# Kernel tuning notes

Hardware: AMD Instinct MI355X
Metric: run time of the kernel (lower is better)

Reference implementation:

```python
import jax, jax.numpy as jnp
import numpy as np

B, S, D, H = 2, 2048, 1024, 16
DK = D // H


def setup_inputs() -> dict:
    key = jax.random.key(0)
    ks = jax.random.split(key, 12)
    scale = 1.0 / np.sqrt(D)
    inp = {
        "q": jax.random.normal(ks[0], (B, S, D), dtype=jnp.float32),
        "k": jax.random.normal(ks[1], (B, S, D), dtype=jnp.float32),
        "v": jax.random.normal(ks[2], (B, S, D), dtype=jnp.float32),
        # causal mask, broadcast over batch and heads; 0 -> masked
        "mask": jnp.tril(jnp.ones((S, S), dtype=jnp.int32))[None, None, :, :],
        "wq_w": jax.random.normal(ks[3], (D, D), dtype=jnp.float32) * scale,
        "wq_b": jax.random.normal(ks[4], (D,), dtype=jnp.float32) * scale,
        "wk_w": jax.random.normal(ks[5], (D, D), dtype=jnp.float32) * scale,
        "wk_b": jax.random.normal(ks[6], (D,), dtype=jnp.float32) * scale,
        "wv_w": jax.random.normal(ks[7], (D, D), dtype=jnp.float32) * scale,
        "wv_b": jax.random.normal(ks[8], (D,), dtype=jnp.float32) * scale,
        "wo_w": jax.random.normal(ks[9], (D, D), dtype=jnp.float32) * scale,
        "wo_b": jax.random.normal(ks[10], (D,), dtype=jnp.float32) * scale,
    }
    return inp


def _split_heads(x):
    b, s, _ = x.shape
    return x.reshape(b, s, H, DK).transpose(0, 2, 1, 3)  # [B,H,S,DK]


def reference(q, k, v, mask, wq_w, wq_b, wk_w, wk_b, wv_w, wv_b, wo_w, wo_b):
    Q = _split_heads(q @ wq_w.T + wq_b)
    K = _split_heads(k @ wk_w.T + wk_b)
    V = _split_heads(v @ wv_w.T + wv_b)
    scale = 1.0 / jnp.sqrt(jnp.asarray(DK, dtype=Q.dtype))
    scores = jnp.einsum("bhqd,bhkd->bhqk", Q, K) * scale  # [B,H,S,S]
    scores = jnp.where(mask == 0, jnp.asarray(-1e9, dtype=scores.dtype), scores)
    attn = jax.nn.softmax(scores, axis=-1)
    out = jnp.einsum("bhqk,bhkd->bhqd", attn, V)  # [B,H,S,DK]
    out = out.transpose(0, 2, 1, 3).reshape(out.shape[0], -1, D)  # [B,S,D]
    return out @ wo_w.T + wo_b
```

## Files before the change

### kernel.cpp

```cpp
#include <hip/hip_runtime.h>
#include <hip/hip_bf16.h>

#define B_ 2
#define S_ 2048
#define D_ 1024
#define H_ 16
#define DK_ 64
#define M_ (B_*S_)

typedef __bf16 bf16;
typedef __bf16 bf16x8 __attribute__((ext_vector_type(8)));
typedef __bf16 bf16x4 __attribute__((ext_vector_type(4)));
typedef float  f32x4  __attribute__((ext_vector_type(4)));

#define GLOAD_LDS16(gp, lp) __builtin_amdgcn_global_load_lds( \
    (const __attribute__((address_space(1))) void*)(gp),      \
    (__attribute__((address_space(3))) void*)(lp), 16, 0, 0)

__global__ __launch_bounds__(256) void cast_kernel(
    const float* __restrict__ q, const float* __restrict__ k, const float* __restrict__ v,
    const float* __restrict__ wq, const float* __restrict__ wk,
    const float* __restrict__ wv, const float* __restrict__ wo,
    bf16* __restrict__ dst)
{
  const size_t XN = (size_t)M_ * D_;
  const size_t WN = (size_t)D_ * D_;
  size_t e = ((size_t)blockIdx.x * 256 + threadIdx.x) * 8;
  const float* src; size_t off;
  if (e < XN)        { src = q; off = e; }
  else if (e < 2*XN) { src = k; off = e - XN; }
  else if (e < 3*XN) { src = v; off = e - 2*XN; }
  else {
    size_t w = e - 3*XN; size_t wi = w >> 20; off = w & (WN - 1);
    src = (wi == 0) ? wq : (wi == 1) ? wk : (wi == 2) ? wv : wo;
  }
  float4 a = *reinterpret_cast<const float4*>(src + off);
  float4 b = *reinterpret_cast<const float4*>(src + off + 4);
  bf16x8 o;
  o[0]=(bf16)a.x; o[1]=(bf16)a.y; o[2]=(bf16)a.z; o[3]=(bf16)a.w;
  o[4]=(bf16)b.x; o[5]=(bf16)b.y; o[6]=(bf16)b.z; o[7]=(bf16)b.w;
  *reinterpret_cast<bf16x8*>(dst + e) = o;
}

__device__ __forceinline__ void gemm_mainloop_128(
    const bf16* __restrict__ A, const bf16* __restrict__ W,
    int m0, int n0, int Kdim, bf16* As, bf16* Bs, f32x4 acc[4][4])
{
  const int tid  = threadIdx.x;
  const int lane = tid & 63;
  const int wave = tid >> 6;
  const int wr   = wave >> 1;
  const int wc   = wave & 1;
  const int g    = lane >> 4;
  const int c    = lane & 15;

#pragma unroll
  for (int i = 0; i < 4; ++i)
#pragma unroll
    for (int j = 0; j < 4; ++j)
      acc[i][j] = (f32x4){0.f, 0.f, 0.f, 0.f};

  for (int kt = 0; kt < Kdim; kt += 32) {
    __syncthreads();
#pragma unroll
    for (int u = 0; u < 2; ++u) {
      int ch  = tid + u*256;
      int row = ch >> 2;
      int col = (ch & 3) * 8;
      GLOAD_LDS16(A + (size_t)(m0 + row)*Kdim + kt + col, As + ch*8);
      GLOAD_LDS16(W + (size_t)(n0 + row)*Kdim + kt + col, Bs + ch*8);
    }
    __syncthreads();

    bf16x8 af[4], bw[4];
#pragma unroll
    for (int i = 0; i < 4; ++i)
      af[i] = *reinterpret_cast<const bf16x8*>(As + (wr*64 + i*16 + c)*32 + g*8);
#pragma unroll
    for (int j = 0; j < 4; ++j)
      bw[j] = *reinterpret_cast<const bf16x8*>(Bs + (wc*64 + j*16 + c)*32 + g*8);
#pragma unroll
    for (int i = 0; i < 4; ++i)
#pragma unroll
      for (int j = 0; j < 4; ++j)
        acc[i][j] = __builtin_amdgcn_mfma_f32_16x16x32_bf16(af[i], bw[j], acc[i][j], 0, 0, 0);
  }
}

__global__ __launch_bounds__(256) void gemm_qkv_kernel(
    const bf16* __restrict__ X, const bf16* __restrict__ Wb,
    const float* __restrict__ bq, const float* __restrict__ bk, const float* __restrict__ bv,
    bf16* __restrict__ Qo, bf16* __restrict__ Ko, bf16* __restrict__ Vo)
{
  __shared__ bf16 As[128*32];
  __shared__ bf16 Bs[128*32];
  const int z  = blockIdx.z;
  const int m0 = blockIdx.y * 128;
  const int n0 = blockIdx.x * 128;
  const bf16* A = X  + (size_t)z * ((size_t)M_ * D_);
  const bf16* W = Wb + (size_t)z * ((size_t)D_ * D_);
  const float* bias = (z == 0) ? bq : (z == 1) ? bk : bv;

  f32x4 acc[4][4];
  gemm_mainloop_128(A, W, m0, n0, D_, As, Bs, acc);

  const int lane = threadIdx.x & 63;
  const int wave = threadIdx.x >> 6;
  const int wr = wave >> 1, wc = wave & 1;
  const int g = lane >> 4,  c = lane & 15;
  bf16* dstQK = (z == 0) ? Qo : Ko;

#pragma unroll
  for (int i = 0; i < 4; ++i) {
#pragma unroll
    for (int j = 0; j < 4; ++j) {
      const int n  = n0 + wc*64 + j*16 + c;
      const float bn = bias[n];
      const int h = n >> 6, dk = n & 63;
      const int mrow = m0 + wr*64 + i*16 + g*4;
      if (z == 2) {
        const int b = mrow >> 11, s = mrow & 2047;
        bf16x4 pv;
#pragma unroll
        for (int r = 0; r < 4; ++r) pv[r] = (bf16)(acc[i][j][r] + bn);
        *reinterpret_cast<bf16x4*>(Vo + ((size_t)((b*H_ + h)*DK_ + dk))*S_ + s) = pv;
      } else {
#pragma unroll
        for (int r = 0; r < 4; ++r) {
          const int m = mrow + r;
          const int b = m >> 11, s = m & 2047;
          dstQK[((size_t)((b*H_ + h)*S_ + s))*DK_ + dk] = (bf16)(acc[i][j][r] + bn);
        }
      }
    }
  }
}

__global__ __launch_bounds__(256) void gemm_out_kernel(
    const bf16* __restrict__ A, const bf16* __restrict__ W,
    const float* __restrict__ bias, float* __restrict__ out)
{
  __shared__ bf16 As[128*32];
  __shared__ bf16 Bs[128*32];
  const int m0 = blockIdx.y * 128;
  const int n0 = blockIdx.x * 128;

  f32x4 acc[4][4];
  gemm_mainloop_128(A, W, m0, n0, D_, As, Bs, acc);

  const int lane = threadIdx.x & 63;
  const int wave = threadIdx.x >> 6;
  const int wr = wave >> 1, wc = wave & 1;
  const int g = lane >> 4,  c = lane & 15;

#pragma unroll
  for (int i = 0; i < 4; ++i) {
#pragma unroll
    for (int j = 0; j < 4; ++j) {
      const int n = n0 + wc*64 + j*16 + c;
      const float bn = bias[n];
      const int mrow = m0 + wr*64 + i*16 + g*4;
#pragma unroll
      for (int r = 0; r < 4; ++r)
        out[(size_t)(mrow + r)*D_ + n] = acc[i][j][r] + bn;
    }
  }
}

__global__ __launch_bounds__(256) void attn_kernel(
    const bf16* __restrict__ Q, const bf16* __restrict__ K,
    const bf16* __restrict__ Vt, bf16* __restrict__ O)
{
  const int qt   = (int)gridDim.x - 1 - (int)blockIdx.x;
  const int bh   = blockIdx.y;
  const int b    = bh >> 4;
  const int hh   = bh & 15;
  const int q0   = qt * 128;
  const int tid  = threadIdx.x;
  const int wave = tid >> 6;
  const int lane = tid & 63;
  const int g    = lane >> 4;
  const int c    = lane & 15;

  __shared__ bf16 Kt_lds[64*64];
  __shared__ bf16 Vt_lds[64*64];
  __shared__ bf16 P_lds[4][32*64];

  const bf16* Qh = Q  + (size_t)bh * (S_*DK_);
  const bf16* Kh = K  + (size_t)bh * (S_*DK_);
  const bf16* Vh = Vt + (size_t)bh * (DK_*S_);

  const int qw0 = q0 + wave*32;

  bf16x8 qfrag[2][2];
#pragma unroll
  for (int qf = 0; qf < 2; ++qf)
#pragma unroll
    for (int ch = 0; ch < 2; ++ch)
      qfrag[qf][ch] = *reinterpret_cast<const bf16x8*>(
          Qh + (size_t)(qw0 + qf*16 + c)*DK_ + ch*32 + g*8);

  f32x4 o_[2][4];
#pragma unroll
  for (int qf = 0; qf < 2; ++qf)
#pragma unroll
    for (int d = 0; d < 4; ++d)
      o_[qf][d] = (f32x4){0.f, 0.f, 0.f, 0.f};
  float m_st[2] = {-1e30f, -1e30f};
  float l_st[2] = {0.f, 0.f};

  const float SC = 0.18033688011112042f;

  const int ntiles = q0/64 + 2;
  const int qmaxw  = qw0 + 31;

  for (int t = 0; t < ntiles; ++t) {
    const int kv0 = t * 64;
    __syncthreads();
#pragma unroll
    for (int u = 0; u < 2; ++u) {
      int ch  = tid + u*256;
      int row = ch >> 3;
      int ssl = (ch & 7) ^ (row & 7);
      GLOAD_LDS16(Kh + (size_t)(kv0 + row)*DK_ + ssl*8, Kt_lds + ch*8);
      GLOAD_LDS16(Vh + (size_t)row*S_ + kv0 + ssl*8,    Vt_lds + ch*8);
    }
    __syncthreads();

    if (kv0 <= qmaxw) {
      f32x4 st[4][2];
#pragma unroll
      for (int kvf = 0; kvf < 4; ++kvf)
#pragma unroll
        for (int qf = 0; qf < 2; ++qf)
          st[kvf][qf] = (f32x4){0.f, 0.f, 0.f, 0.f};

#pragma unroll
      for (int kvf = 0; kvf < 4; ++kvf) {
        const int kvr = kvf*16 + c;
        bf16x8 kf[2];
#pragma unroll
        for (int ch = 0; ch < 2; ++ch) {
          int off = kvr*128 + (((ch*4 + g) ^ (kvr & 7)) << 4);
          kf[ch] = *reinterpret_cast<const bf16x8*>(
              reinterpret_cast<const char*>(Kt_lds) + off);
        }
#pragma unroll
        for (int qf = 0; qf < 2; ++qf)
#pragma unroll
          for (int ch = 0; ch < 2; ++ch)
            st[kvf][qf] = __builtin_amdgcn_mfma_f32_16x16x32_bf16(
                kf[ch], qfrag[qf][ch], st[kvf][qf], 0, 0, 0);
      }

#pragma unroll
      for (int qf = 0; qf < 2; ++qf) {
        const int qrow = qw0 + qf*16 + c;
        float mloc = -1e30f;
#pragma unroll
        for (int kvf = 0; kvf < 4; ++kvf)
#pragma unroll
          for (int r = 0; r < 4; ++r) {
            const int kv = kv0 + kvf*16 + g*4 + r;
            float vv = st[kvf][qf][r] * SC;
            vv = (kv <= qrow) ? vv : -1e30f;
            st[kvf][qf][r] = vv;
            mloc = fmaxf(mloc, vv);
          }
        mloc = fmaxf(mloc, __shfl_xor(mloc, 16));
        mloc = fmaxf(mloc, __shfl_xor(mloc, 32));
        const float mnew = fmaxf(m_st[qf], mloc);
        const float corr = exp2f(m_st[qf] - mnew);
        float lsum = 0.f;
        const int q_l = qf*16 + c;
#pragma unroll
        for (int kvf = 0; kvf < 4; ++kvf) {
          bf16x4 pb;
#pragma unroll
          for (int r = 0; r < 4; ++r) {
            float p = exp2f(st[kvf][qf][r] - mnew);
            lsum += p;
            pb[r] = (bf16)p;
          }
          int wb = (q_l*128 + kvf*32 + g*8) ^ ((q_l & 7) << 4);
          *reinterpret_cast<bf16x4*>(reinterpret_cast<char*>(P_lds[wave]) + wb) = pb;
        }
        lsum += __shfl_xor(lsum, 16);
        lsum += __shfl_xor(lsum, 32);
        l_st[qf] = l_st[qf]*corr + lsum;
        m_st[qf] = mnew;
#pragma unroll
        for (int r = 0; r < 4; ++r) {
          float rc = __shfl(corr, (lane & 48) | (g*4 + r));
#pragma unroll
          for (int d = 0; d < 4; ++d)
            o_[qf][d][r] *= rc;
        }
      }

      bf16x8 pf[2][2];
#pragma unroll
      for (int qf = 0; qf < 2; ++qf) {
        const int q_l = qf*16 + c;
#pragma unroll
        for (int ch = 0; ch < 2; ++ch) {
          int rb = (q_l*128 + ch*64 + g*16) ^ ((q_l & 7) << 4);
          pf[qf][ch] = *reinterpret_cast<const bf16x8*>(
              reinterpret_cast<const char*>(P_lds[wave]) + rb);
        }
      }
#pragma unroll
      for (int d = 0; d < 4; ++d) {
        const int dkr = d*16 + c;
#pragma unroll
        for (int ch = 0; ch < 2; ++ch) {
          int vb = dkr*128 + (((ch*4 + g) ^ (dkr & 7)) << 4);
          bf16x8 vf = *reinterpret_cast<const bf16x8*>(
              reinterpret_cast<const char*>(Vt_lds) + vb);
#pragma unroll
          for (int qf = 0; qf < 2; ++qf)
            o_[qf][d] = __builtin_amdgcn_mfma_f32_16x16x32_bf16(
                pf[qf][ch], vf, o_[qf][d], 0, 0, 0);
        }
      }
    }
  }

#pragma unroll
  for (int qf = 0; qf < 2; ++qf) {
    const float linv = 1.f / l_st[qf];
#pragma unroll
    for (int r = 0; r < 4; ++r) {
      const float li = __shfl(linv, (lane & 48) | (g*4 + r));
      const int qrow = qw0 + qf*16 + g*4 + r;
      bf16* orow = O + ((size_t)(b*S_ + qrow)*H_ + hh)*DK_;
#pragma unroll
      for (int d = 0; d < 4; ++d)
        orow[d*16 + c] = (bf16)(o_[qf][d][r] * li);
    }
  }
}

extern "C" void kernel_launch(void* const* d_in, const int* in_sizes, int n_in,
                              void* d_out, int out_size, void* d_ws, size_t ws_size,
                              hipStream_t stream)
{
  const float* q    = (const float*)d_in[0];
  const float* k    = (const float*)d_in[1];
  const float* v    = (const float*)d_in[2];
  const float* wq_w = (const float*)d_in[4];
  const float* wq_b = (const float*)d_in[5];
  const float* wk_w = (const float*)d_in[6];
  const float* wk_b = (const float*)d_in[7];
  const float* wv_w = (const float*)d_in[8];
  const float* wv_b = (const float*)d_in[9];
  const float* wo_w = (const float*)d_in[10];
  const float* wo_b = (const float*)d_in[11];

  const size_t XN = (size_t)M_ * D_;
  const size_t WN = (size_t)D_ * D_;
  bf16* ws  = (bf16*)d_ws;
  bf16* xq  = ws;
  bf16* wqb = ws + 3*XN;
  bf16* Qs  = wqb + 4*WN;
  bf16* Ks  = Qs + XN;
  bf16* Vts = Ks + XN;
  bf16* Os  = ws;

  cast_kernel<<<dim3(8192), dim3(256), 0, stream>>>(q, k, v, wq_w, wk_w, wv_w, wo_w, xq);
  gemm_qkv_kernel<<<dim3(8, 32, 3), dim3(256), 0, stream>>>(
      xq, wqb, wq_b, wk_b, wv_b, Qs, Ks, Vts);
  attn_kernel<<<dim3(16, 32), dim3(256), 0, stream>>>(Qs, Ks, Vts, Os);
  gemm_out_kernel<<<dim3(8, 32), dim3(256), 0, stream>>>(Os, wqb + 3*WN, wo_b, (float*)d_out);
}
```

Before: 285.4 us.

## Rewrite attention with 32x32 MFMA, register-resident P, and double-buffered KV

Reworks the attention kernel to use 32x32x16 MFMA tiles, with each lane owning one query row. The softmax probabilities are repacked into MFMA operands with cross-lane shuffles instead of a round trip through LDS. K/V tiles are double-buffered so the next tile's global-to-LDS load overlaps the current compute, leaving one barrier per iteration. The softmax scale is folded into the Q projection epilogue, the causal masking is skipped for tiles fully below the diagonal, and a launch bound of two blocks per unit is set. In exchange it doubles LDS for K/V and uses a finite -30000 mask value.

After: 267.7 us. 6.2% less time.

```diff
diff --git a/kernel.cpp b/kernel.cpp
--- a/kernel.cpp
+++ b/kernel.cpp
@@ -11,11 +11,19 @@
 typedef __bf16 bf16;
 typedef __bf16 bf16x8 __attribute__((ext_vector_type(8)));
 typedef __bf16 bf16x4 __attribute__((ext_vector_type(4)));
+typedef __bf16 bf16x2 __attribute__((ext_vector_type(2)));
 typedef float  f32x4  __attribute__((ext_vector_type(4)));
+typedef float  f32x16 __attribute__((ext_vector_type(16)));
+typedef int    i32x4  __attribute__((ext_vector_type(4)));
 
 #define GLOAD_LDS16(gp, lp) __builtin_amdgcn_global_load_lds( \
     (const __attribute__((address_space(1))) void*)(gp),      \
     (__attribute__((address_space(3))) void*)(lp), 16, 0, 0)
+
+static __device__ __forceinline__ int packbf(float a, float b) {
+  bf16x2 t; t[0] = (bf16)a; t[1] = (bf16)b;
+  return __builtin_bit_cast(int, t);
+}
 
 __global__ __launch_bounds__(256) void cast_kernel(
     const float* __restrict__ q, const float* __restrict__ k, const float* __restrict__ v,
@@ -100,6 +108,7 @@
   const bf16* A = X  + (size_t)z * ((size_t)M_ * D_);
   const bf16* W = Wb + (size_t)z * ((size_t)D_ * D_);
   const float* bias = (z == 0) ? bq : (z == 1) ? bk : bv;
+  const float sc = (z == 0) ? 0.18033688011112042f : 1.0f;
 
   f32x4 acc[4][4];
   gemm_mainloop_128(A, W, m0, n0, D_, As, Bs, acc);
@@ -129,7 +138,7 @@
         for (int r = 0; r < 4; ++r) {
           const int m = mrow + r;
           const int b = m >> 11, s = m & 2047;
-          dstQK[((size_t)((b*H_ + h)*S_ + s))*DK_ + dk] = (bf16)(acc[i][j][r] + bn);
+          dstQK[((size_t)((b*H_ + h)*S_ + s))*DK_ + dk] = (bf16)((acc[i][j][r] + bn) * sc);
         }
       }
     }
@@ -167,7 +176,7 @@
   }
 }
 
-__global__ __launch_bounds__(256) void attn_kernel(
+__global__ __launch_bounds__(256, 2) void attn_kernel(
     const bf16* __restrict__ Q, const bf16* __restrict__ K,
     const bf16* __restrict__ Vt, bf16* __restrict__ O)
 {
@@ -179,166 +188,150 @@
   const int tid  = threadIdx.x;
   const int wave = tid >> 6;
   const int lane = tid & 63;
-  const int g    = lane >> 4;
-  const int c    = lane & 15;
-
-  __shared__ bf16 Kt_lds[64*64];
-  __shared__ bf16 Vt_lds[64*64];
-  __shared__ bf16 P_lds[4][32*64];
+  const int ql   = lane & 31;
+  const int hi   = lane >> 5;
+
+  const float NEG = -30000.0f;
+
+  __shared__ bf16 Kl[2][64*64];
+  __shared__ bf16 Vl[2][64*64];
 
   const bf16* Qh = Q  + (size_t)bh * (S_*DK_);
   const bf16* Kh = K  + (size_t)bh * (S_*DK_);
   const bf16* Vh = Vt + (size_t)bh * (DK_*S_);
 
-  const int qw0 = q0 + wave*32;
-
-  bf16x8 qfrag[2][2];
-#pragma unroll
-  for (int qf = 0; qf < 2; ++qf)
-#pragma unroll
-    for (int ch = 0; ch < 2; ++ch)
-      qfrag[qf][ch] = *reinterpret_cast<const bf16x8*>(
-          Qh + (size_t)(qw0 + qf*16 + c)*DK_ + ch*32 + g*8);
-
-  f32x4 o_[2][4];
-#pragma unroll
-  for (int qf = 0; qf < 2; ++qf)
-#pragma unroll
-    for (int d = 0; d < 4; ++d)
-      o_[qf][d] = (f32x4){0.f, 0.f, 0.f, 0.f};
-  float m_st[2] = {-1e30f, -1e30f};
-  float l_st[2] = {0.f, 0.f};
-
-  const float SC = 0.18033688011112042f;
-
-  const int ntiles = q0/64 + 2;
-  const int qmaxw  = qw0 + 31;
-
-  for (int t = 0; t < ntiles; ++t) {
+  const int qw0  = q0 + wave*32;
+  const int qrow = qw0 + ql;
+
+  bf16x8 qf[4];
+#pragma unroll
+  for (int ck = 0; ck < 4; ++ck)
+    qf[ck] = *reinterpret_cast<const bf16x8*>(Qh + (size_t)qrow*DK_ + ck*16 + hi*8);
+
+  f32x16 o0 = {}, o1 = {};
+  float m_ = 0.f, l_ = 0.f;
+
+  const int nt = q0/64 + 2;
+
+#define STAGE_KV(kv0s, bb) do {                                              \
+  _Pragma("unroll")                                                          \
+  for (int u = 0; u < 2; ++u) {                                              \
+    int ch  = tid + u*256;                                                   \
+    int row = ch >> 3;                                                       \
+    int g   = (ch & 7) ^ (row & 7);            \
+    GLOAD_LDS16(Kh + (size_t)((kv0s) + row)*DK_ + g*8, &Kl[bb][ch*8]);       \
+    GLOAD_LDS16(Vh + (size_t)row*S_ + (kv0s) + g*8,    &Vl[bb][ch*8]);       \
+  }                                                                          \
+} while (0)
+
+#define MK_PA(dst, s, base) do {                                               \
+    int x0 = packbf(s[(base)+0], s[(base)+1]);                                 \
+    int x1 = packbf(s[(base)+2], s[(base)+3]);                                 \
+    int y0 = packbf(s[(base)+4], s[(base)+5]);                                 \
+    int y1 = packbf(s[(base)+6], s[(base)+7]);                                 \
+    int px0 = __shfl_xor(x0, 32), px1 = __shfl_xor(x1, 32);                    \
+    int py0 = __shfl_xor(y0, 32), py1 = __shfl_xor(y1, 32);                    \
+    i32x4 w;                                                                   \
+    w[0] = hi ? py0 : x0;  w[1] = hi ? py1 : x1;                               \
+    w[2] = hi ? y0  : px0; w[3] = hi ? y1  : px1;                              \
+    dst = __builtin_bit_cast(bf16x8, w);                                       \
+  } while (0)
+
+  int cur = 0;
+  STAGE_KV(0, 0);
+  __syncthreads();
+
+  for (int t = 0; t < nt; ++t) {
     const int kv0 = t * 64;
+    if (t + 1 < nt) STAGE_KV((t+1)*64, cur ^ 1);
+
+    if (kv0 <= qw0 + 31) {
+      const char* Kb = (const char*)Kl[cur];
+      const char* Vb = (const char*)Vl[cur];
+
+      f32x16 st0 = {}, st1 = {};
+#pragma unroll
+      for (int ck = 0; ck < 4; ++ck) {
+        bf16x8 kf0 = *reinterpret_cast<const bf16x8*>(
+            Kb + ql*128 + (((ck*2 + hi) ^ (ql & 7)) << 4));
+        st0 = __builtin_amdgcn_mfma_f32_32x32x16_bf16(kf0, qf[ck], st0, 0, 0, 0);
+        bf16x8 kf1 = *reinterpret_cast<const bf16x8*>(
+            Kb + (32 + ql)*128 + (((ck*2 + hi) ^ (ql & 7)) << 4));
+        st1 = __builtin_amdgcn_mfma_f32_32x32x16_bf16(kf1, qf[ck], st1, 0, 0, 0);
+      }
+
+      if (kv0 + 63 > qw0) {
+#pragma unroll
+        for (int r = 0; r < 16; ++r) {
+          const int kvr = kv0 + (r & 3) + 8*(r >> 2) + 4*hi;
+          st0[r] = (kvr      <= qrow) ? st0[r] : NEG;
+          st1[r] = (kvr + 32 <= qrow) ? st1[r] : NEG;
+        }
+      }
+
+      float pm = st0[0];
+#pragma unroll
+      for (int r = 1; r < 16; ++r) pm = fmaxf(pm, st0[r]);
+#pragma unroll
+      for (int r = 0; r < 16; ++r) pm = fmaxf(pm, st1[r]);
+      pm = fmaxf(pm, __shfl_xor(pm, 32));
+
+      const float mnew = fmaxf(m_, pm);
+      const float corr = exp2f(m_ - mnew);
+      m_ = mnew;
+
+      float ls = 0.f;
+#pragma unroll
+      for (int r = 0; r < 16; ++r) {
+        float p = exp2f(st0[r] - mnew);
+        ls += p;
+        st0[r] = p;
+      }
+#pragma unroll
+      for (int r = 0; r < 16; ++r) {
+        float p = exp2f(st1[r] - mnew);
+        ls += p;
+        st1[r] = p;
+      }
+      l_ = l_ * corr + (ls + __shfl_xor(ls, 32));
+      o0 *= corr; o1 *= corr;
+
+      bf16x8 pa[4];
+      MK_PA(pa[0], st0, 0);
+      MK_PA(pa[1], st0, 8);
+      MK_PA(pa[2], st1, 0);
+      MK_PA(pa[3], st1, 8);
+
+#pragma unroll
+      for (int ck = 0; ck < 4; ++ck) {
+        bf16x8 vf0 = *reinterpret_cast<const bf16x8*>(
+            Vb + ql*128 + (((ck*2 + hi) ^ (ql & 7)) << 4));
+        o0 = __builtin_amdgcn_mfma_f32_32x32x16_bf16(vf0, pa[ck], o0, 0, 0, 0);
+        bf16x8 vf1 = *reinterpret_cast<const bf16x8*>(
+            Vb + (32 + ql)*128 + (((ck*2 + hi) ^ (ql & 7)) << 4));
+        o1 = __builtin_amdgcn_mfma_f32_32x32x16_bf16(vf1, pa[ck], o1, 0, 0, 0);
+      }
+    }
+
     __syncthreads();
-#pragma unroll
-    for (int u = 0; u < 2; ++u) {
-      int ch  = tid + u*256;
-      int row = ch >> 3;
-      int ssl = (ch & 7) ^ (row & 7);
-      GLOAD_LDS16(Kh + (size_t)(kv0 + row)*DK_ + ssl*8, Kt_lds + ch*8);
-      GLOAD_LDS16(Vh + (size_t)row*S_ + kv0 + ssl*8,    Vt_lds + ch*8);
-    }
-    __syncthreads();
-
-    if (kv0 <= qmaxw) {
-      f32x4 st[4][2];
-#pragma unroll
-      for (int kvf = 0; kvf < 4; ++kvf)
-#pragma unroll
-        for (int qf = 0; qf < 2; ++qf)
-          st[kvf][qf] = (f32x4){0.f, 0.f, 0.f, 0.f};
-
-#pragma unroll
-      for (int kvf = 0; kvf < 4; ++kvf) {
-        const int kvr = kvf*16 + c;
-        bf16x8 kf[2];
-#pragma unroll
-        for (int ch = 0; ch < 2; ++ch) {
-          int off = kvr*128 + (((ch*4 + g) ^ (kvr & 7)) << 4);
-          kf[ch] = *reinterpret_cast<const bf16x8*>(
-              reinterpret_cast<const char*>(Kt_lds) + off);
-        }
-#pragma unroll
-        for (int qf = 0; qf < 2; ++qf)
-#pragma unroll
-          for (int ch = 0; ch < 2; ++ch)
-            st[kvf][qf] = __builtin_amdgcn_mfma_f32_16x16x32_bf16(
-                kf[ch], qfrag[qf][ch], st[kvf][qf], 0, 0, 0);
-      }
-
-#pragma unroll
-      for (int qf = 0; qf < 2; ++qf) {
-        const int qrow = qw0 + qf*16 + c;
-        float mloc = -1e30f;
-#pragma unroll
-        for (int kvf = 0; kvf < 4; ++kvf)
-#pragma unroll
-          for (int r = 0; r < 4; ++r) {
-            const int kv = kv0 + kvf*16 + g*4 + r;
-            float vv = st[kvf][qf][r] * SC;
-            vv = (kv <= qrow) ? vv : -1e30f;
-            st[kvf][qf][r] = vv;
-            mloc = fmaxf(mloc, vv);
-          }
-        mloc = fmaxf(mloc, __shfl_xor(mloc, 16));
-        mloc = fmaxf(mloc, __shfl_xor(mloc, 32));
-        const float mnew = fmaxf(m_st[qf], mloc);
-        const float corr = exp2f(m_st[qf] - mnew);
-        float lsum = 0.f;
-        const int q_l = qf*16 + c;
-#pragma unroll
-        for (int kvf = 0; kvf < 4; ++kvf) {
-          bf16x4 pb;
-#pragma unroll
-          for (int r = 0; r < 4; ++r) {
-            float p = exp2f(st[kvf][qf][r] - mnew);
-            lsum += p;
-            pb[r] = (bf16)p;
-          }
-          int wb = (q_l*128 + kvf*32 + g*8) ^ ((q_l & 7) << 4);
-          *reinterpret_cast<bf16x4*>(reinterpret_cast<char*>(P_lds[wave]) + wb) = pb;
-        }
-        lsum += __shfl_xor(lsum, 16);
-        lsum += __shfl_xor(lsum, 32);
-        l_st[qf] = l_st[qf]*corr + lsum;
-        m_st[qf] = mnew;
-#pragma unroll
-        for (int r = 0; r < 4; ++r) {
-          float rc = __shfl(corr, (lane & 48) | (g*4 + r));
-#pragma unroll
-          for (int d = 0; d < 4; ++d)
-            o_[qf][d][r] *= rc;
-        }
-      }
-
-      bf16x8 pf[2][2];
-#pragma unroll
-      for (int qf = 0; qf < 2; ++qf) {
-        const int q_l = qf*16 + c;
-#pragma unroll
-        for (int ch = 0; ch < 2; ++ch) {
-          int rb = (q_l*128 + ch*64 + g*16) ^ ((q_l & 7) << 4);
-          pf[qf][ch] = *reinterpret_cast<const bf16x8*>(
-              reinterpret_cast<const char*>(P_lds[wave]) + rb);
-        }
-      }
-#pragma unroll
-      for (int d = 0; d < 4; ++d) {
-        const int dkr = d*16 + c;
-#pragma unroll
-        for (int ch = 0; ch < 2; ++ch) {
-          int vb = dkr*128 + (((ch*4 + g) ^ (dkr & 7)) << 4);
-          bf16x8 vf = *reinterpret_cast<const bf16x8*>(
-              reinterpret_cast<const char*>(Vt_lds) + vb);
-#pragma unroll
-          for (int qf = 0; qf < 2; ++qf)
-            o_[qf][d] = __builtin_amdgcn_mfma_f32_16x16x32_bf16(
-                pf[qf][ch], vf, o_[qf][d], 0, 0, 0);
-        }
-      }
-    }
-  }
-
-#pragma unroll
-  for (int qf = 0; qf < 2; ++qf) {
-    const float linv = 1.f / l_st[qf];
-#pragma unroll
-    for (int r = 0; r < 4; ++r) {
-      const float li = __shfl(linv, (lane & 48) | (g*4 + r));
-      const int qrow = qw0 + qf*16 + g*4 + r;
-      bf16* orow = O + ((size_t)(b*S_ + qrow)*H_ + hh)*DK_;
-#pragma unroll
-      for (int d = 0; d < 4; ++d)
-        orow[d*16 + c] = (bf16)(o_[qf][d][r] * li);
-    }
-  }
+    cur ^= 1;
+  }
+
+  const float linv = 1.0f / l_;
+  bf16* orow = O + ((size_t)(b*S_ + qrow)*H_ + hh)*DK_;
+#pragma unroll
+  for (int w4 = 0; w4 < 4; ++w4) {
+    bf16x4 s0, s1;
+#pragma unroll
+    for (int e = 0; e < 4; ++e) {
+      s0[e] = (bf16)(o0[w4*4 + e] * linv);
+      s1[e] = (bf16)(o1[w4*4 + e] * linv);
+    }
+    *reinterpret_cast<bf16x4*>(orow + 8*w4 + 4*hi)      = s0;
+    *reinterpret_cast<bf16x4*>(orow + 32 + 8*w4 + 4*hi) = s1;
+  }
+#undef STAGE_KV
+#undef MK_PA
 }
 
 extern "C" void kernel_launch(void* const* d_in, const int* in_sizes, int n_in,
```
